# Kernel optimization log

Hardware: AMD Instinct MI355X
Metric: run time of the kernel (lower is better)

## Reference

```python
import jax, jax.numpy as jnp
import numpy as np

B, N = 4096, 128


def setup_inputs() -> dict:
    key = jax.random.key(0)
    X = jax.random.normal(key, (B, N, N), dtype=jnp.float32)
    # SPD batch: X X^T / N + eps*I guarantees strictly positive eigenvalues
    spd = jnp.einsum('bij,bkj->bik', X, X) / N + 1e-3 * jnp.eye(N, dtype=jnp.float32)[None]
    return {"input": spd}


def reference(input) -> jnp.ndarray:
    # Batched eigendecomposition (symmetric input -> eigh), then v @ diag(log e) @ v^T
    e, v = jnp.linalg.eigh(input)          # e: [B, N], v: [B, N, N]
    return jnp.einsum('bij,bj,bkj->bik', v, jnp.log(e), v)
```

## Files before the change

### kernel.cpp

```cpp
#include <hip/hip_runtime.h>
#include <hip/hip_bf16.h>
#include <math.h>

#define NM   128
#define PAD  132
#define PB   136

typedef __attribute__((ext_vector_type(8))) short bf16x8;
typedef __attribute__((ext_vector_type(4))) float f32x4;


__global__ __launch_bounds__(256,1)
void scale_kernel(const float* __restrict__ A, float* __restrict__ outY,
                  float* __restrict__ outM, float* __restrict__ lns)
{
    __shared__ __align__(16) float L[NM][PAD];
    __shared__ float rs[NM];
    __shared__ float s_inv;
    const int t = threadIdx.x;
    const long long b = blockIdx.x;
    const long long off = b << 14;
    for (int v = 0; v < 16; ++v) {
        int f = t + v*256;
        int row = f >> 5, c4 = (f & 31) << 2;
        *(float4*)&L[row][c4] = ((const float4*)(A + off))[f];
    }
    __syncthreads();
    if (t < NM) {
        float s = 0.f;
        for (int j = 0; j < NM; ++j) s += fabsf(L[t][j]);
        rs[t] = s;
    }
    __syncthreads();
    if (t < 64) {
        float m = fmaxf(rs[t], rs[t+64]);
        #pragma unroll
        for (int o = 32; o > 0; o >>= 1) m = fmaxf(m, __shfl_down(m, o, 64));
        if (t == 0) { s_inv = 1.0f/m; lns[b] = logf(m); }
    }
    __syncthreads();
    const float inv = s_inv;
    for (int v = 0; v < 16; ++v) {
        int f = t + v*256;
        int row = f >> 5, c4 = (f & 31) << 2;
        float4 x = *(const float4*)&L[row][c4];
        x.x *= inv; x.y *= inv; x.z *= inv; x.w *= inv;
        ((float4*)(outY + off))[f] = x;
        ((float4*)(outM + off))[f] = x;
    }
}

__global__ __launch_bounds__(256,1)
void rescale_kernel(const float* __restrict__ Sq, float* __restrict__ X,
                    float* __restrict__ M, float* __restrict__ lns)
{
    __shared__ __align__(16) float L[NM][PAD];
    __shared__ float rs[NM];
    __shared__ float s_g;
    const int t = threadIdx.x;
    const long long b = blockIdx.x;
    const long long off = b << 14;
    for (int v = 0; v < 16; ++v) {
        int f = t + v*256;
        int row = f >> 5, c4 = (f & 31) << 2;
        *(float4*)&L[row][c4] = ((const float4*)(Sq + off))[f];
    }
    __syncthreads();
    if (t < NM) {
        float s = 0.f;
        for (int j = 0; j < NM; ++j) s += fabsf(L[t][j]);
        rs[t] = s;
    }
    __syncthreads();
    if (t < 64) {
        float m = fmaxf(rs[t], rs[t+64]);
        #pragma unroll
        for (int o = 32; o > 0; o >>= 1) m = fmaxf(m, __shfl_down(m, o, 64));
        if (t == 0) { s_g = 1.0f/sqrtf(m); lns[b] = lns[b] + 0.5f*logf(m); }
    }
    __syncthreads();
    const float g = s_g;
    for (int v = 0; v < 16; ++v) {
        int f = t + v*256;
        float4 x = ((const float4*)(X + off))[f];
        x.x *= g; x.y *= g; x.z *= g; x.w *= g;
        ((float4*)(X + off))[f] = x;
        ((float4*)(M + off))[f] = x;
    }
}

__device__ __forceinline__ void tridec(int u, int &bi, int &bj) {
    int b = (int)(0.5f*(sqrtf(8.0f*(float)u + 1.0f) - 1.0f));
    while ((b+1)*(b+2)/2 <= u) ++b;
    while (b*(b+1)/2 > u) --b;
    bi = b; bj = u - b*(b+1)/2;
}

__global__ __launch_bounds__(512,1)
void gram_tri(const float* __restrict__ X, float* __restrict__ Out)
{
    __shared__ __align__(16) float LX[NM][PAD];
    const int t = threadIdx.x;
    const long long off = (long long)blockIdx.x << 14;
    for (int v = 0; v < 8; ++v) {
        int f = t + v*512;
        int row = f >> 5, c4 = (f & 31) << 2;
        *(float4*)&LX[row][c4] = ((const float4*)(X + off))[f];
    }
    __syncthreads();
    for (int u = t; u < 528; u += 512) {
        int bi, bj; tridec(u, bi, bj);
        const int r4 = bi << 2, c4 = bj << 2;
        float acc[4][4];
        #pragma unroll
        for (int i = 0; i < 4; ++i)
            #pragma unroll
            for (int j = 0; j < 4; ++j) acc[i][j] = 0.f;
        #pragma unroll 4
        for (int k = 0; k < NM; ++k) {
            float av[4], bv[4];
            *(float4*)av = *(const float4*)&LX[k][r4];
            *(float4*)bv = *(const float4*)&LX[k][c4];
            #pragma unroll
            for (int i = 0; i < 4; ++i)
                #pragma unroll
                for (int j = 0; j < 4; ++j) acc[i][j] = fmaf(av[i], bv[j], acc[i][j]);
        }
        #pragma unroll
        for (int i = 0; i < 4; ++i)
            *(float4*)&Out[off + (long long)(r4+i)*NM + c4] =
                make_float4(acc[i][0], acc[i][1], acc[i][2], acc[i][3]);
        if (bi != bj) {
            #pragma unroll
            for (int j = 0; j < 4; ++j)
                *(float4*)&Out[off + (long long)(c4+j)*NM + r4] =
                    make_float4(acc[0][j], acc[1][j], acc[2][j], acc[3][j]);
        }
    }
}

__device__ __forceinline__ void tri_p1_reg(const float (*LM)[PAD], const float (*LY)[PAD],
                                           int bi, int bj, float a15, float a05,
                                           float o[4][4])
{
    const int r4 = bi << 2, c4 = bj << 2;
    float acc[4][4];
    #pragma unroll
    for (int i = 0; i < 4; ++i)
        #pragma unroll
        for (int j = 0; j < 4; ++j) acc[i][j] = 0.f;
    #pragma unroll 4
    for (int k = 0; k < NM; ++k) {
        float av[4], bv[4];
        *(float4*)av = *(const float4*)&LY[k][r4];
        *(float4*)bv = *(const float4*)&LM[k][c4];
        #pragma unroll
        for (int i = 0; i < 4; ++i)
            #pragma unroll
            for (int j = 0; j < 4; ++j) acc[i][j] = fmaf(av[i], bv[j], acc[i][j]);
    }
    #pragma unroll
    for (int i = 0; i < 4; ++i)
        #pragma unroll
        for (int j = 0; j < 4; ++j)
            o[i][j] = a15*LY[r4+i][c4+j] - a05*acc[i][j];
    if (bi == bj) {
        #pragma unroll
        for (int i = 0; i < 4; ++i)
            #pragma unroll
            for (int j = 0; j < 4; ++j)
                if (j > i) { float s = 0.5f*(o[i][j] + o[j][i]); o[i][j] = s; o[j][i] = s; }
    }
}

__device__ __forceinline__ void tri_p2_lds(const float (*LM)[PAD], float (*LY)[PAD],
                                           int bi, int bj)
{
    const int r4 = bi << 2, c4 = bj << 2;
    float acc[4][4];
    #pragma unroll
    for (int i = 0; i < 4; ++i)
        #pragma unroll
        for (int j = 0; j < 4; ++j) acc[i][j] = 0.f;
    #pragma unroll 4
    for (int k = 0; k < NM; ++k) {
        float av[4], bv[4];
        *(float4*)av = *(const float4*)&LM[k][r4];
        *(float4*)bv = *(const float4*)&LM[k][c4];
        #pragma unroll
        for (int i = 0; i < 4; ++i)
            #pragma unroll
            for (int j = 0; j < 4; ++j) acc[i][j] = fmaf(av[i], bv[j], acc[i][j]);
    }
    #pragma unroll
    for (int i = 0; i < 4; ++i)
        *(float4*)&LY[r4+i][c4] = make_float4(acc[i][0], acc[i][1], acc[i][2], acc[i][3]);
    if (bi != bj) {
        #pragma unroll
        for (int j = 0; j < 4; ++j)
            *(float4*)&LY[c4+j][r4] = make_float4(acc[0][j], acc[1][j], acc[2][j], acc[3][j]);
    }
}

__device__ __forceinline__ void tri_p3_reg(const float (*LM)[PAD], const float (*LY)[PAD],
                                           int bi, int bj, float q, float o[4][4])
{
    const int r4 = bi << 2, c4 = bj << 2;
    float acc[4][4];
    #pragma unroll
    for (int i = 0; i < 4; ++i)
        #pragma unroll
        for (int j = 0; j < 4; ++j) acc[i][j] = 0.f;
    #pragma unroll 4
    for (int k = 0; k < NM; ++k) {
        float av[4], bv[4];
        *(float4*)av = *(const float4*)&LM[k][r4];
        *(float4*)bv = *(const float4*)&LY[k][c4];
        #pragma unroll
        for (int i = 0; i < 4; ++i)
            #pragma unroll
            for (int j = 0; j < 4; ++j) acc[i][j] = fmaf(av[i], bv[j], acc[i][j]);
    }
    #pragma unroll
    for (int i = 0; i < 4; ++i)
        #pragma unroll
        for (int j = 0; j < 4; ++j)
            o[i][j] = q*(9.f*LM[r4+i][c4+j] - 6.f*LY[r4+i][c4+j] + acc[i][j]);
    if (bi == bj) {
        #pragma unroll
        for (int i = 0; i < 4; ++i)
            #pragma unroll
            for (int j = 0; j < 4; ++j)
                if (j > i) { float s = 0.5f*(o[i][j] + o[j][i]); o[i][j] = s; o[j][i] = s; }
    }
}

__device__ __forceinline__ void tri_wb(float (*L)[PAD], int bi, int bj, const float o[4][4])
{
    const int r4 = bi << 2, c4 = bj << 2;
    #pragma unroll
    for (int i = 0; i < 4; ++i)
        *(float4*)&L[r4+i][c4] = make_float4(o[i][0], o[i][1], o[i][2], o[i][3]);
    if (bi != bj) {
        #pragma unroll
        for (int j = 0; j < 4; ++j)
            *(float4*)&L[c4+j][r4] = make_float4(o[0][j], o[1][j], o[2][j], o[3][j]);
    }
}

__global__ __launch_bounds__(512,1)
void ns_tri4(const float* __restrict__ Mp, const float* __restrict__ Yp,
             float* __restrict__ outM, float* __restrict__ outY, int niter)
{
    __shared__ __align__(16) float LM[NM][PAD];
    __shared__ __align__(16) float LY[NM][PAD];
    const int t = threadIdx.x;
    const long long off = (long long)blockIdx.x << 14;
    for (int v = 0; v < 8; ++v) {
        int f = t + v*512;
        int row = f >> 5, c4 = (f & 31) << 2;
        *(float4*)&LM[row][c4] = ((const float4*)(Mp + off))[f];
        *(float4*)&LY[row][c4] = ((const float4*)(Yp + off))[f];
    }
    __syncthreads();

    int b0i, b0j, b1i = -1, b1j = 0;
    tridec(t, b0i, b0j);
    if (t < 16) tridec(512 + t, b1i, b1j);

    const float cc = 1.5f, dd = sqrtf(1.5f);
    const float a15 = 1.5f*dd, a05 = 0.5f*dd, q = 0.25f*cc;
    float y0[4][4], y1[4][4], m0[4][4], m1[4][4];

    for (int it = 0; it < niter; ++it) {
        tri_p1_reg(LM, LY, b0i, b0j, a15, a05, y0);
        if (b1i >= 0) tri_p1_reg(LM, LY, b1i, b1j, a15, a05, y1);
        __syncthreads();
        tri_p2_lds(LM, LY, b0i, b0j);
        if (b1i >= 0) tri_p2_lds(LM, LY, b1i, b1j);
        __syncthreads();
        tri_p3_reg(LM, LY, b0i, b0j, q, m0);
        if (b1i >= 0) tri_p3_reg(LM, LY, b1i, b1j, q, m1);
        __syncthreads();
        tri_wb(LM, b0i, b0j, m0);
        tri_wb(LY, b0i, b0j, y0);
        if (b1i >= 0) { tri_wb(LM, b1i, b1j, m1); tri_wb(LY, b1i, b1j, y1); }
        __syncthreads();
    }

    for (int v = 0; v < 8; ++v) {
        int f = t + v*512;
        int row = f >> 5, c4 = (f & 31) << 2;
        ((float4*)(outM + off))[f] = *(const float4*)&LM[row][c4];
        ((float4*)(outY + off))[f] = *(const float4*)&LY[row][c4];
    }
}

__device__ __forceinline__ f32x4 mfma16(bf16x8 a, bf16x8 b, f32x4 c) {
    return __builtin_amdgcn_mfma_f32_16x16x32_bf16(a, b, c, 0, 0, 0);
}

__device__ __forceinline__ void splitbf(float x, unsigned short &h, unsigned short &l) {
    __hip_bfloat16 bh = __float2bfloat16(x);
    float r = x - __bfloat162float(bh);
    __hip_bfloat16 bl = __float2bfloat16(r);
    h = *(unsigned short*)&bh;
    l = *(unsigned short*)&bl;
}

__device__ __forceinline__ float ldsM(const unsigned short* __restrict__ H,
                                      const unsigned short* __restrict__ L,
                                      int row, int col) {
    unsigned int uh = ((unsigned int)H[row*PB + col]) << 16;
    unsigned int ul = ((unsigned int)L[row*PB + col]) << 16;
    return __uint_as_float(uh) + __uint_as_float(ul);
}

__device__ __forceinline__ bf16x8 ldfrag(const unsigned short* __restrict__ a,
                                         int rb, int lane, int kc) {
    int row = rb*16 + (lane & 15);
    int col = kc*32 + ((lane >> 4) & 3)*8;
    return *(const bf16x8*)(a + row*PB + col);
}

__device__ __forceinline__ f32x4 symdiag(f32x4 a, int lane) {
    const int g = (lane >> 4) & 3, j = lane & 15;
    const int rp = j & 3;
    f32x4 out;
    #pragma unroll
    for (int r = 0; r < 4; ++r) {
        int lp = 4*g + r + ((j >> 2) << 4);
        float t0 = __shfl(a[0], lp, 64);
        float t1 = __shfl(a[1], lp, 64);
        float t2 = __shfl(a[2], lp, 64);
        float t3 = __shfl(a[3], lp, 64);
        float tv = (rp == 0) ? t0 : (rp == 1) ? t1 : (rp == 2) ? t2 : t3;
        out[r] = 0.5f*(a[r] + tv);
    }
    return out;
}

__device__ __forceinline__ void st_split(unsigned short* __restrict__ H,
                                         unsigned short* __restrict__ L,
                                         int Tr, int Tc, int lane, f32x4 o) {
    int col = Tc*16 + (lane & 15);
    int rb  = Tr*16 + ((lane >> 4) & 3)*4;
    #pragma unroll
    for (int r = 0; r < 4; ++r) {
        unsigned short h, l;
        splitbf(o[r], h, l);
        H[(rb+r)*PB + col] = h;
        L[(rb+r)*PB + col] = l;
        if (Tr != Tc) { H[col*PB + rb + r] = h; L[col*PB + rb + r] = l; }
    }
}

__device__ __forceinline__ void stg_sym(float* __restrict__ out, long long off,
                                        int Tr, int Tc, int lane, f32x4 o) {
    int col = Tc*16 + (lane & 15);
    int rb  = Tr*16 + ((lane >> 4) & 3)*4;
    #pragma unroll
    for (int r = 0; r < 4; ++r)
        out[off + (long long)(rb+r)*NM + col] = o[r];
    if (Tr != Tc)
        *(f32x4*)&out[off + (long long)col*NM + rb] = o;
}

__device__ __forceinline__ f32x4 yepi(const unsigned short* __restrict__ Yh,
                                      const unsigned short* __restrict__ Yl,
                                      int Tr, int Tc, int lane, f32x4 a,
                                      float a15, float a05) {
    int col = Tc*16 + (lane & 15);
    int rb  = Tr*16 + ((lane >> 4) & 3)*4;
    f32x4 o;
    #pragma unroll
    for (int r = 0; r < 4; ++r)
        o[r] = a15*ldsM(Yh, Yl, rb+r, col) - a05*a[r];
    if (Tr == Tc) o = symdiag(o, lane);
    return o;
}

__device__ __forceinline__ f32x4 mepi(const unsigned short* __restrict__ Mh,
                                      const unsigned short* __restrict__ Ml,
                                      const unsigned short* __restrict__ Th,
                                      const unsigned short* __restrict__ Tl,
                                      int Tr, int Tc, int lane, f32x4 a, float q) {
    int col = Tc*16 + (lane & 15);
    int rb  = Tr*16 + ((lane >> 4) & 3)*4;
    f32x4 o;
    #pragma unroll
    for (int r = 0; r < 4; ++r)
        o[r] = q*(9.f*ldsM(Mh, Ml, rb+r, col) - 6.f*ldsM(Th, Tl, rb+r, col) + a[r]);
    if (Tr == Tc) o = symdiag(o, lane);
    return o;
}

__device__ __forceinline__ f32x4 pepi(const unsigned short* __restrict__ Ph,
                                      const unsigned short* __restrict__ Pl,
                                      int Tr, int Tc, int lane, f32x4 a,
                                      float s1, float s2, float dadd) {
    int col = Tc*16 + (lane & 15);
    int rb  = Tr*16 + ((lane >> 4) & 3)*4;
    f32x4 o;
    #pragma unroll
    for (int r = 0; r < 4; ++r)
        o[r] = s1*a[r] - s2*ldsM(Ph, Pl, rb+r, col) + ((rb+r) == col ? dadd : 0.f);
    if (Tr == Tc) o = symdiag(o, lane);
    return o;
}

template<int W>
struct TS16 {
    static constexpr int P  = W >> 2;
    static constexpr int Q  = W & 3;
    static constexpr int R0 = P;
    static constexpr int R1 = 7 - P;
    static constexpr int N  = (Q == 0) ? 3 : 2;
    static constexpr int g(int i)  { return 4*i + Q; }
    static constexpr int tr(int i) { return g(i) <= R0 ? R0 : R1; }
    static constexpr int tc(int i) { return g(i) <= R0 ? g(i) : g(i) - R0 - 1; }
};

template<int W>
__device__ __forceinline__ void tri16_gemm(const unsigned short* __restrict__ Ah,
                                           const unsigned short* __restrict__ Al,
                                           const unsigned short* __restrict__ Bh,
                                           const unsigned short* __restrict__ Bl,
                                           int lane, f32x4* acc) {
    using TS = TS16<W>;
    #pragma unroll
    for (int kc = 0; kc < 4; ++kc) {
        bf16x8 a0h = ldfrag(Ah, TS::R0, lane, kc), a0l = ldfrag(Al, TS::R0, lane, kc);
        bf16x8 a1h = ldfrag(Ah, TS::R1, lane, kc), a1l = ldfrag(Al, TS::R1, lane, kc);
        #pragma unroll
        for (int i = 0; i < TS::N; ++i) {
            const int r = TS::tr(i), c = TS::tc(i);
            bf16x8 bh = ldfrag(Bh, c, lane, kc), bl = ldfrag(Bl, c, lane, kc);
            bf16x8 ah = (r == TS::R0) ? a0h : a1h;
            bf16x8 al = (r == TS::R0) ? a0l : a1l;
            acc[i] = mfma16(ah, bh, acc[i]);
            acc[i] = mfma16(ah, bl, acc[i]);
            acc[i] = mfma16(al, bh, acc[i]);
        }
    }
}

template<int W>
__device__ __forceinline__ void ns_fused_body16(
    unsigned short* Mh, unsigned short* Ml,
    unsigned short* Yh, unsigned short* Yl,
    float* outY, long long off, int lane, int niter)
{
    using TS = TS16<W>;
    constexpr int NT_ = TS::N;
    const f32x4 z = {0.f, 0.f, 0.f, 0.f};
    f32x4 acc[NT_], yv[NT_];

    for (int j = 0; j < niter; ++j) {
        const int last = (j == niter-1);
        const float cc = (j < niter-3) ? 1.5f : ((j == niter-3) ? 1.116f : 1.0f);
        const float dd = sqrtf(cc);
        const float a15 = 1.5f*dd, a05 = 0.5f*dd;

        #pragma unroll
        for (int i = 0; i < NT_; ++i) acc[i] = z;
        tri16_gemm<W>(Yh, Yl, Mh, Ml, lane, acc);
        #pragma unroll
        for (int i = 0; i < NT_; ++i)
            yv[i] = yepi(Yh, Yl, TS::tr(i), TS::tc(i), lane, acc[i], a15, a05);

        if (last) {
            #pragma unroll
            for (int i = 0; i < NT_; ++i)
                stg_sym(outY, off, TS::tr(i), TS::tc(i), lane, yv[i]);
            return;
        }
        __syncthreads();

        #pragma unroll
        for (int i = 0; i < NT_; ++i) acc[i] = z;
        tri16_gemm<W>(Mh, Ml, Mh, Ml, lane, acc);
        #pragma unroll
        for (int i = 0; i < NT_; ++i)
            st_split(Yh, Yl, TS::tr(i), TS::tc(i), lane, acc[i]);
        __syncthreads();

        #pragma unroll
        for (int i = 0; i < NT_; ++i) acc[i] = z;
        tri16_gemm<W>(Mh, Ml, Yh, Yl, lane, acc);
        const float q = 0.25f*cc;
        #pragma unroll
        for (int i = 0; i < NT_; ++i)
            acc[i] = mepi(Mh, Ml, Yh, Yl, TS::tr(i), TS::tc(i), lane, acc[i], q);
        __syncthreads();

        #pragma unroll
        for (int i = 0; i < NT_; ++i)
            st_split(Mh, Ml, TS::tr(i), TS::tc(i), lane, acc[i]);
        #pragma unroll
        for (int i = 0; i < NT_; ++i)
            st_split(Yh, Yl, TS::tr(i), TS::tc(i), lane, yv[i]);
        __syncthreads();
    }
}

__global__ __launch_bounds__(1024,1)
void ns_fused(const float* __restrict__ Mp, const float* __restrict__ Yp,
              float* __restrict__ outY, int niter)
{
    __shared__ __align__(16) unsigned short pool[4*NM*PB];
    unsigned short* Mh = pool;
    unsigned short* Ml = pool + NM*PB;
    unsigned short* Yh = pool + 2*NM*PB;
    unsigned short* Yl = pool + 3*NM*PB;

    const int t = threadIdx.x;
    const long long off = (long long)blockIdx.x << 14;
    for (int v = 0; v < 4; ++v) {
        int f = t + v*1024;
        int row = f >> 5, c4 = (f & 31) << 2;
        float4 x = ((const float4*)(Mp + off))[f];
        ushort4 h, l;
        splitbf(x.x, h.x, l.x); splitbf(x.y, h.y, l.y);
        splitbf(x.z, h.z, l.z); splitbf(x.w, h.w, l.w);
        *(ushort4*)&Mh[row*PB + c4] = h;
        *(ushort4*)&Ml[row*PB + c4] = l;
        x = ((const float4*)(Yp + off))[f];
        splitbf(x.x, h.x, l.x); splitbf(x.y, h.y, l.y);
        splitbf(x.z, h.z, l.z); splitbf(x.w, h.w, l.w);
        *(ushort4*)&Yh[row*PB + c4] = h;
        *(ushort4*)&Yl[row*PB + c4] = l;
    }
    __syncthreads();

    const int lane = t & 63;
    const int w = t >> 6;
    switch (w) {
        case 0:  ns_fused_body16<0>(Mh,Ml,Yh,Yl,outY,off,lane,niter); break;
        case 1:  ns_fused_body16<1>(Mh,Ml,Yh,Yl,outY,off,lane,niter); break;
        case 2:  ns_fused_body16<2>(Mh,Ml,Yh,Yl,outY,off,lane,niter); break;
        case 3:  ns_fused_body16<3>(Mh,Ml,Yh,Yl,outY,off,lane,niter); break;
        case 4:  ns_fused_body16<4>(Mh,Ml,Yh,Yl,outY,off,lane,niter); break;
        case 5:  ns_fused_body16<5>(Mh,Ml,Yh,Yl,outY,off,lane,niter); break;
        case 6:  ns_fused_body16<6>(Mh,Ml,Yh,Yl,outY,off,lane,niter); break;
        case 7:  ns_fused_body16<7>(Mh,Ml,Yh,Yl,outY,off,lane,niter); break;
        case 8:  ns_fused_body16<8>(Mh,Ml,Yh,Yl,outY,off,lane,niter); break;
        case 9:  ns_fused_body16<9>(Mh,Ml,Yh,Yl,outY,off,lane,niter); break;
        case 10: ns_fused_body16<10>(Mh,Ml,Yh,Yl,outY,off,lane,niter); break;
        case 11: ns_fused_body16<11>(Mh,Ml,Yh,Yl,outY,off,lane,niter); break;
        case 12: ns_fused_body16<12>(Mh,Ml,Yh,Yl,outY,off,lane,niter); break;
        case 13: ns_fused_body16<13>(Mh,Ml,Yh,Yl,outY,off,lane,niter); break;
        case 14: ns_fused_body16<14>(Mh,Ml,Yh,Yl,outY,off,lane,niter); break;
        default: ns_fused_body16<15>(Mh,Ml,Yh,Yl,outY,off,lane,niter); break;
    }
}

struct PolyCoefs {
    float a, bd;
    float s1, s2;
    float c0,c1,c2,c3,c4,c5;
    float f1, f2, f3;
};

template<int W>
__device__ __forceinline__ void poly_fused_body16(
    const unsigned short* Xh, const unsigned short* Xl,
    unsigned short* Ph, unsigned short* Pl,
    float* Out, long long off, int lane, PolyCoefs pc, float lnsb)
{
    using TS = TS16<W>;
    constexpr int NT_ = TS::N;
    const f32x4 z = {0.f, 0.f, 0.f, 0.f};
    f32x4 acc[NT_];

    for (int step = 0; step < 6; ++step) {
        #pragma unroll
        for (int i = 0; i < NT_; ++i) acc[i] = z;
        tri16_gemm<W>(Xh, Xl, Ph, Pl, lane, acc);
        float s3v;
        switch (step) {
            case 0: s3v = pc.c0; break;  case 1: s3v = pc.c1; break;
            case 2: s3v = pc.c2; break;  case 3: s3v = pc.c3; break;
            case 4: s3v = pc.c4; break;  default: s3v = pc.c5; break;
        }
        #pragma unroll
        for (int i = 0; i < NT_; ++i)
            acc[i] = pepi(Ph, Pl, TS::tr(i), TS::tc(i), lane, acc[i], pc.s1, pc.s2, s3v);
        __syncthreads();
        #pragma unroll
        for (int i = 0; i < NT_; ++i)
            st_split(Ph, Pl, TS::tr(i), TS::tc(i), lane, acc[i]);
        __syncthreads();
    }
    #pragma unroll
    for (int i = 0; i < NT_; ++i) acc[i] = z;
    tri16_gemm<W>(Xh, Xl, Ph, Pl, lane, acc);
    const float dadd = pc.f3 + lnsb;
    #pragma unroll
    for (int i = 0; i < NT_; ++i) {
        f32x4 o = pepi(Ph, Pl, TS::tr(i), TS::tc(i), lane, acc[i], pc.f1, pc.f2, dadd);
        stg_sym(Out, off, TS::tr(i), TS::tc(i), lane, o);
    }
}

__global__ __launch_bounds__(1024,1)
void poly_fused(const float* __restrict__ Xp, float* __restrict__ Out,
                const float* __restrict__ lns, PolyCoefs pc)
{
    __shared__ __align__(16) unsigned short pool[4*NM*PB];
    unsigned short* Xh = pool;
    unsigned short* Xl = pool + NM*PB;
    unsigned short* Ph = pool + 2*NM*PB;
    unsigned short* Pl = pool + 3*NM*PB;

    const int t = threadIdx.x;
    const long long b = blockIdx.x;
    const long long off = b << 14;
    for (int v = 0; v < 4; ++v) {
        int f = t + v*1024;
        int row = f >> 5, c4 = (f & 31) << 2;
        float4 x = ((const float4*)(Xp + off))[f];
        float4 p;
        p.x = pc.a*x.x + ((c4+0)==row ? pc.bd : 0.f);
        p.y = pc.a*x.y + ((c4+1)==row ? pc.bd : 0.f);
        p.z = pc.a*x.z + ((c4+2)==row ? pc.bd : 0.f);
        p.w = pc.a*x.w + ((c4+3)==row ? pc.bd : 0.f);
        ushort4 h, l;
        splitbf(x.x, h.x, l.x); splitbf(x.y, h.y, l.y);
        splitbf(x.z, h.z, l.z); splitbf(x.w, h.w, l.w);
        *(ushort4*)&Xh[row*PB + c4] = h;
        *(ushort4*)&Xl[row*PB + c4] = l;
        splitbf(p.x, h.x, l.x); splitbf(p.y, h.y, l.y);
        splitbf(p.z, h.z, l.z); splitbf(p.w, h.w, l.w);
        *(ushort4*)&Ph[row*PB + c4] = h;
        *(ushort4*)&Pl[row*PB + c4] = l;
    }
    __syncthreads();

    const float lnsb = lns[b];
    const int lane = t & 63;
    const int w = t >> 6;
    switch (w) {
        case 0:  poly_fused_body16<0>(Xh,Xl,Ph,Pl,Out,off,lane,pc,lnsb); break;
        case 1:  poly_fused_body16<1>(Xh,Xl,Ph,Pl,Out,off,lane,pc,lnsb); break;
        case 2:  poly_fused_body16<2>(Xh,Xl,Ph,Pl,Out,off,lane,pc,lnsb); break;
        case 3:  poly_fused_body16<3>(Xh,Xl,Ph,Pl,Out,off,lane,pc,lnsb); break;
        case 4:  poly_fused_body16<4>(Xh,Xl,Ph,Pl,Out,off,lane,pc,lnsb); break;
        case 5:  poly_fused_body16<5>(Xh,Xl,Ph,Pl,Out,off,lane,pc,lnsb); break;
        case 6:  poly_fused_body16<6>(Xh,Xl,Ph,Pl,Out,off,lane,pc,lnsb); break;
        case 7:  poly_fused_body16<7>(Xh,Xl,Ph,Pl,Out,off,lane,pc,lnsb); break;
        case 8:  poly_fused_body16<8>(Xh,Xl,Ph,Pl,Out,off,lane,pc,lnsb); break;
        case 9:  poly_fused_body16<9>(Xh,Xl,Ph,Pl,Out,off,lane,pc,lnsb); break;
        case 10: poly_fused_body16<10>(Xh,Xl,Ph,Pl,Out,off,lane,pc,lnsb); break;
        case 11: poly_fused_body16<11>(Xh,Xl,Ph,Pl,Out,off,lane,pc,lnsb); break;
        case 12: poly_fused_body16<12>(Xh,Xl,Ph,Pl,Out,off,lane,pc,lnsb); break;
        case 13: poly_fused_body16<13>(Xh,Xl,Ph,Pl,Out,off,lane,pc,lnsb); break;
        case 14: poly_fused_body16<14>(Xh,Xl,Ph,Pl,Out,off,lane,pc,lnsb); break;
        default: poly_fused_body16<15>(Xh,Xl,Ph,Pl,Out,off,lane,pc,lnsb); break;
    }
}

#define LDA  129
#define NT   512
#define MAX_SWEEPS 14

__global__ __launch_bounds__(NT, 1)
void logeig_jacobi(const float* __restrict__ in, float* __restrict__ out)
{
    __shared__ float A[NM][LDA];
    __shared__ float V[NM][LDA];
    __shared__ float rc[64], rs[64];
    __shared__ float logd[NM];
    __shared__ float roff[NT/64], rdia[NT/64];
    __shared__ int   s_done;

    const int t = threadIdx.x;
    const long long b = blockIdx.x;
    const float* __restrict__ Ain  = in  + (b << 14);
    float* __restrict__       Aout = out + (b << 14);

    for (int k = 0; k < (NM*NM)/NT; ++k) {
        int idx = t + k*NT;
        int i = idx >> 7, j = idx & 127;
        A[i][j] = Ain[idx];
        V[i][j] = (i == j) ? 1.0f : 0.0f;
    }
    __syncthreads();

    for (int sweep = 0; sweep < MAX_SWEEPS; ++sweep) {
        for (int r = 0; r < NM-1; ++r) {
            if (t < 64) {
                int m = t, p, q;
                if (m == 0) { p = NM-1; q = r; }
                else {
                    p = r + m;            if (p >= NM-1) p -= (NM-1);
                    q = r - m + (NM-1);   if (q >= NM-1) q -= (NM-1);
                }
                float app = A[p][p], aqq = A[q][q], apq = A[p][q];
                float c = 1.0f, s = 0.0f;
                if (fabsf(apq) > 1e-12f*(fabsf(app)+fabsf(aqq)) + 1e-32f) {
                    float tau = (aqq - app) * 0.5f / apq;
                    float tt  = 1.0f / (fabsf(tau) + sqrtf(fmaf(tau,tau,1.0f)));
                    tt = (tau < 0.0f) ? -tt : tt;
                    c = rsqrtf(fmaf(tt,tt,1.0f));
                    s = tt * c;
                }
                rc[m] = c; rs[m] = s;
            }
            __syncthreads();
            for (int k = 0; k < (2*64*NM)/NT; ++k) {
                int task = t + k*NT;
                int i   = task & 127;
                int m   = (task >> 7) & 63;
                int isV = task >> 13;
                int p, q;
                if (m == 0) { p = NM-1; q = r; }
                else {
                    p = r + m;            if (p >= NM-1) p -= (NM-1);
                    q = r - m + (NM-1);   if (q >= NM-1) q -= (NM-1);
                }
                float c = rc[m], s = rs[m];
                if (isV == 0) {
                    float x = A[i][p], y = A[i][q];
                    A[i][p] = c*x - s*y;
                    A[i][q] = s*x + c*y;
                } else {
                    float x = V[i][p], y = V[i][q];
                    V[i][p] = c*x - s*y;
                    V[i][q] = s*x + c*y;
                }
            }
            __syncthreads();
            for (int k = 0; k < (64*NM)/NT; ++k) {
                int task = t + k*NT;
                int j = task & 127;
                int m = task >> 7;
                int p, q;
                if (m == 0) { p = NM-1; q = r; }
                else {
                    p = r + m;            if (p >= NM-1) p -= (NM-1);
                    q = r - m + (NM-1);   if (q >= NM-1) q -= (NM-1);
                }
                float c = rc[m], s = rs[m];
                float x = A[p][j], y = A[q][j];
                A[p][j] = c*x - s*y;
                A[q][j] = s*x + c*y;
            }
            __syncthreads();
        }
        float off2 = 0.0f, dia2 = 0.0f;
        for (int k = 0; k < (NM*NM)/NT; ++k) {
            int idx = t + k*NT;
            int i = idx >> 7, j = idx & 127;
            float v = A[i][j];
            if (i == j) dia2 += v*v; else off2 += v*v;
        }
        #pragma unroll
        for (int o = 32; o > 0; o >>= 1) {
            off2 += __shfl_down(off2, o, 64);
            dia2 += __shfl_down(dia2, o, 64);
        }
        if ((t & 63) == 0) { roff[t >> 6] = off2; rdia[t >> 6] = dia2; }
        __syncthreads();
        if (t == 0) {
            float o2 = 0.0f, d2 = 0.0f;
            for (int w = 0; w < NT/64; ++w) { o2 += roff[w]; d2 += rdia[w]; }
            s_done = (o2 <= 1e-13f * d2) ? 1 : 0;
        }
        __syncthreads();
        if (s_done) break;
    }

    if (t < NM) logd[t] = logf(fmaxf(A[t][t], 1e-12f));
    __syncthreads();
    for (int kk = 0; kk < (NM*NM)/NT; ++kk) {
        int idx = t + kk*NT;
        int i = idx >> 7, k = idx & 127;
        A[i][k] = V[i][k] * logd[k];
    }
    __syncthreads();
    {
        int i  = t >> 2;
        int jb = t & 3;
        float acc[32];
        #pragma unroll
        for (int jj = 0; jj < 32; ++jj) acc[jj] = 0.0f;
        for (int kk = 0; kk < NM; ++kk) {
            int k = (kk + jb) & 127;
            float w = A[i][k];
            #pragma unroll
            for (int jj = 0; jj < 32; ++jj)
                acc[jj] = fmaf(w, V[jb*32 + jj][k], acc[jj]);
        }
        #pragma unroll
        for (int jj = 0; jj < 32; ++jj)
            Aout[i*NM + jb*32 + jj] = acc[jj];
    }
}

static void cheb_log_power(double lo, double up, int deg, double* p)
{
    const int NC = deg + 1;
    const int MN = 64;
    double mid = 0.5*(lo+up), hw = 0.5*(up-lo);
    double cc[32];
    for (int j = 0; j < NC; ++j) {
        double s = 0.0;
        for (int m = 0; m < MN; ++m) {
            double th = M_PI*(m+0.5)/MN;
            s += log(mid + hw*cos(th)) * cos(j*th);
        }
        cc[j] = 2.0*s/MN;
    }
    double Tp[32] = {0}, Tc[32] = {0}, Tn[32];
    for (int j = 0; j < NC; ++j) p[j] = 0.0;
    Tp[0] = 1.0;  p[0] += 0.5*cc[0];
    Tc[1] = 1.0;  p[1] += cc[1];
    for (int k = 2; k <= deg; ++k) {
        for (int j = 0; j < NC; ++j) Tn[j] = -Tp[j];
        for (int j = 1; j < NC; ++j) Tn[j] += 2.0*Tc[j-1];
        for (int j = 0; j < NC; ++j) { p[j] += cc[k]*Tn[j]; Tp[j] = Tc[j]; Tc[j] = Tn[j]; }
    }
}

extern "C" void kernel_launch(void* const* d_in, const int* in_sizes, int n_in,
                              void* d_out, int out_size, void* d_ws, size_t ws_size,
                              hipStream_t stream) {
    const float* in = (const float*)d_in[0];
    float* out = (float*)d_out;
    const int batch = in_sizes[0] >> 14;
    const size_t matBytes = (size_t)batch * NM * NM * 4;
    const size_t need = matBytes + (size_t)batch * 4;

    if (ws_size < need) {
        logeig_jacobi<<<batch, NT, 0, stream>>>(in, out);
        return;
    }

    float* Mbuf = (float*)d_ws;
    float* lns  = (float*)((char*)d_ws + matBytes);

    scale_kernel<<<batch, 256, 0, stream>>>(in, out, Mbuf, lns);
    gram_tri<<<batch, 512, 0, stream>>>(out, Mbuf);
    rescale_kernel<<<batch, 256, 0, stream>>>(Mbuf, out, Mbuf, lns);

    ns_tri4<<<batch, 512, 0, stream>>>(Mbuf, out, Mbuf, out, 4);

    ns_fused<<<batch, 1024, 0, stream>>>(Mbuf, out, out, 8);
    ns_fused<<<batch, 1024, 0, stream>>>(out,  out, out, 8);
    ns_fused<<<batch, 1024, 0, stream>>>(out,  out, out, 6);

    const double lo = 0.25, up = 1.002;
    const double mid = 0.5*(lo+up), hw = 0.5*(up-lo);
    double p[9];
    cheb_log_power(lo, up, 8, p);

    PolyCoefs pc;
    pc.a  = (float)(p[8]/hw);
    pc.bd = (float)(p[7] - p[8]*mid/hw);
    pc.s1 = (float)(1.0/hw);
    pc.s2 = (float)(mid/hw);
    pc.c0 = (float)p[6]; pc.c1 = (float)p[5]; pc.c2 = (float)p[4];
    pc.c3 = (float)p[3]; pc.c4 = (float)p[2]; pc.c5 = (float)p[1];
    pc.f1 = (float)(8.0/hw);
    pc.f2 = (float)(8.0*mid/hw);
    pc.f3 = (float)(8.0*p[0]);

    poly_fused<<<batch, 1024, 0, stream>>>(out, out, lns, pc);
}
```

Before: 7.207 ms.

## Run first Newton-Schulz stage with int8 MFMA using three-way fixed-point split

Adds an ns_i8 kernel that encodes M and Y as 24-bit fixed-point values split into three int8 planes in LDS. The triangular Newton-Schulz GEMMs then run as eight int8 16x16x64 MFMAs per tile, reconstructed in fp32. It replaces ns_tri4 for the first four iterations when the int8 MFMA builtin is available. The aim is to use the higher int8 matrix throughput in place of the bf16 split path. In exchange it adds fixed-point quantization, which assumes values stay within a bounded range, plus extra packing and unpacking work.

```diff
diff --git a/kernel.cpp b/kernel.cpp
--- a/kernel.cpp
+++ b/kernel.cpp
@@ -5,9 +5,17 @@
 #define NM   128
 #define PAD  132
 #define PB   136
+#define PBI  144
 
 typedef __attribute__((ext_vector_type(8))) short bf16x8;
 typedef __attribute__((ext_vector_type(4))) float f32x4;
+typedef __attribute__((ext_vector_type(4))) int   i32x4;
+
+#if defined(__has_builtin)
+#if __has_builtin(__builtin_amdgcn_mfma_i32_16x16x64_i8)
+#define HAVE_I8MFMA 1
+#endif
+#endif
 
 
 __global__ __launch_bounds__(256,1)
@@ -659,6 +667,259 @@
         default: poly_fused_body16<15>(Xh,Xl,Ph,Pl,Out,off,lane,pc,lnsb); break;
     }
 }
+
+#if HAVE_I8MFMA
+
+__device__ __forceinline__ i32x4 mfma8(i32x4 a, i32x4 b, i32x4 c) {
+    return __builtin_amdgcn_mfma_i32_16x16x64_i8(a, b, c, 0, 0, 0);
+}
+
+__device__ __forceinline__ void spliti(float x, int &h, int &m, int &l) {
+    int xi = __float2int_rn(x * 2097152.0f);
+    l = (int)(signed char)(xi & 255);
+    int r1 = (xi - l) >> 8;
+    m = (int)(signed char)(r1 & 255);
+    h = (r1 - m) >> 8;
+}
+
+__device__ __forceinline__ void pack4i(float4 x, unsigned &uh, unsigned &um, unsigned &ul) {
+    float v[4] = {x.x, x.y, x.z, x.w};
+    uh = um = ul = 0;
+    #pragma unroll
+    for (int i = 0; i < 4; ++i) {
+        int h, m, l;
+        spliti(v[i], h, m, l);
+        uh |= ((unsigned)(h & 255)) << (8*i);
+        um |= ((unsigned)(m & 255)) << (8*i);
+        ul |= ((unsigned)(l & 255)) << (8*i);
+    }
+}
+
+__device__ __forceinline__ float recLDS(const signed char* __restrict__ H,
+                                        const signed char* __restrict__ Md,
+                                        const signed char* __restrict__ L,
+                                        int row, int col) {
+    int v = ((int)H[row*PBI + col] << 16) + ((int)Md[row*PBI + col] << 8)
+          + (int)L[row*PBI + col];
+    return (float)v * 4.76837158203125e-7f;
+}
+
+__device__ __forceinline__ f32x4 rec4(i32x4 g0, i32x4 g1, i32x4 g2, i32x4 g3) {
+    f32x4 r;
+    #pragma unroll
+    for (int i = 0; i < 4; ++i)
+        r[i] = (float)g0[i]*9.765625e-4f
+             + (float)g1[i]*3.814697265625e-6f
+             + (float)g2[i]*1.4901161193847656e-8f
+             + (float)g3[i]*5.8207660913467407e-11f;
+    return r;
+}
+
+__device__ __forceinline__ i32x4 ldfrag8(const signed char* __restrict__ p,
+                                         int rb, int lane, int kc) {
+    int row = rb*16 + (lane & 15);
+    int col = kc*64 + ((lane >> 4) & 3)*16;
+    return *(const i32x4*)(p + row*PBI + col);
+}
+
+__device__ __forceinline__ void st_spliti(signed char* __restrict__ H,
+                                          signed char* __restrict__ Md,
+                                          signed char* __restrict__ L,
+                                          int Tr, int Tc, int lane, f32x4 o) {
+    int col = Tc*16 + (lane & 15);
+    int rb  = Tr*16 + ((lane >> 4) & 3)*4;
+    #pragma unroll
+    for (int r = 0; r < 4; ++r) {
+        int h, m, l;
+        spliti(o[r], h, m, l);
+        H[(rb+r)*PBI + col] = (signed char)h;
+        Md[(rb+r)*PBI + col] = (signed char)m;
+        L[(rb+r)*PBI + col] = (signed char)l;
+        if (Tr != Tc) {
+            H[col*PBI + rb + r] = (signed char)h;
+            Md[col*PBI + rb + r] = (signed char)m;
+            L[col*PBI + rb + r] = (signed char)l;
+        }
+    }
+}
+
+template<int W>
+struct TS8 {
+    static constexpr int P  = W & 3;
+    static constexpr int R0 = P;
+    static constexpr int R1 = 7 - P;
+    static constexpr int H  = W >> 2;
+    static constexpr int N  = (10 - H) / 2;
+    static constexpr int tr(int i) { int g = 2*i + H; return g <= R0 ? R0 : R1; }
+    static constexpr int tc(int i) { int g = 2*i + H; return g <= R0 ? g : g - R0 - 1; }
+};
+
+template<int W>
+__device__ __forceinline__ void tri8_gemm_i8(
+    const signed char* __restrict__ Ah, const signed char* __restrict__ Am,
+    const signed char* __restrict__ Al,
+    const signed char* __restrict__ Bh, const signed char* __restrict__ Bm,
+    const signed char* __restrict__ Bl,
+    int lane, i32x4* g0, i32x4* g1, i32x4* g2, i32x4* g3)
+{
+    using TS = TS8<W>;
+    #pragma unroll
+    for (int kc = 0; kc < 2; ++kc) {
+        i32x4 a0h = ldfrag8(Ah, TS::R0, lane, kc);
+        i32x4 a0m = ldfrag8(Am, TS::R0, lane, kc);
+        i32x4 a0l = ldfrag8(Al, TS::R0, lane, kc);
+        i32x4 a1h = ldfrag8(Ah, TS::R1, lane, kc);
+        i32x4 a1m = ldfrag8(Am, TS::R1, lane, kc);
+        i32x4 a1l = ldfrag8(Al, TS::R1, lane, kc);
+        #pragma unroll
+        for (int i = 0; i < TS::N; ++i) {
+            const int r = TS::tr(i), c = TS::tc(i);
+            i32x4 bh = ldfrag8(Bh, c, lane, kc);
+            i32x4 bm = ldfrag8(Bm, c, lane, kc);
+            i32x4 bl = ldfrag8(Bl, c, lane, kc);
+            i32x4 ah = (r == TS::R0) ? a0h : a1h;
+            i32x4 am = (r == TS::R0) ? a0m : a1m;
+            i32x4 al = (r == TS::R0) ? a0l : a1l;
+            g0[i] = mfma8(ah, bh, g0[i]);
+            g1[i] = mfma8(ah, bm, g1[i]);
+            g1[i] = mfma8(am, bh, g1[i]);
+            g2[i] = mfma8(ah, bl, g2[i]);
+            g2[i] = mfma8(am, bm, g2[i]);
+            g2[i] = mfma8(al, bh, g2[i]);
+            g3[i] = mfma8(am, bl, g3[i]);
+            g3[i] = mfma8(al, bm, g3[i]);
+        }
+    }
+}
+
+template<int W>
+__device__ __forceinline__ void ns_i8_body(
+    signed char* Mh, signed char* Mm, signed char* Ml,
+    signed char* Yh, signed char* Ym, signed char* Yl,
+    float* outM, float* outY, long long off, int lane, int niter)
+{
+    using TS = TS8<W>;
+    constexpr int NT_ = TS::N;
+    const i32x4 zi = {0, 0, 0, 0};
+    i32x4 g0[NT_], g1[NT_], g2[NT_], g3[NT_];
+    f32x4 yv[NT_], mv[NT_];
+    const float cc = 1.5f, dd = sqrtf(1.5f);
+    const float a15 = 1.5f*dd, a05 = 0.5f*dd, q = 0.25f*cc;
+
+    for (int j = 0; j < niter; ++j) {
+        const int last = (j == niter-1);
+
+        #pragma unroll
+        for (int i = 0; i < NT_; ++i) { g0[i]=zi; g1[i]=zi; g2[i]=zi; g3[i]=zi; }
+        tri8_gemm_i8<W>(Yh,Ym,Yl, Mh,Mm,Ml, lane, g0,g1,g2,g3);
+        #pragma unroll
+        for (int i = 0; i < NT_; ++i) {
+            f32x4 a = rec4(g0[i], g1[i], g2[i], g3[i]);
+            int Tr = TS::tr(i), Tc = TS::tc(i);
+            int col = Tc*16 + (lane & 15);
+            int rb  = Tr*16 + ((lane >> 4) & 3)*4;
+            f32x4 o;
+            #pragma unroll
+            for (int r = 0; r < 4; ++r)
+                o[r] = a15*recLDS(Yh, Ym, Yl, rb+r, col) - a05*a[r];
+            if (Tr == Tc) o = symdiag(o, lane);
+            yv[i] = o;
+        }
+        __syncthreads();
+
+        #pragma unroll
+        for (int i = 0; i < NT_; ++i) { g0[i]=zi; g1[i]=zi; g2[i]=zi; g3[i]=zi; }
+        tri8_gemm_i8<W>(Mh,Mm,Ml, Mh,Mm,Ml, lane, g0,g1,g2,g3);
+        #pragma unroll
+        for (int i = 0; i < NT_; ++i) {
+            f32x4 tv = rec4(g0[i], g1[i], g2[i], g3[i]);
+            st_spliti(Yh, Ym, Yl, TS::tr(i), TS::tc(i), lane, tv);
+        }
+        __syncthreads();
+
+        #pragma unroll
+        for (int i = 0; i < NT_; ++i) { g0[i]=zi; g1[i]=zi; g2[i]=zi; g3[i]=zi; }
+        tri8_gemm_i8<W>(Mh,Mm,Ml, Yh,Ym,Yl, lane, g0,g1,g2,g3);
+        #pragma unroll
+        for (int i = 0; i < NT_; ++i) {
+            f32x4 a = rec4(g0[i], g1[i], g2[i], g3[i]);
+            int Tr = TS::tr(i), Tc = TS::tc(i);
+            int col = Tc*16 + (lane & 15);
+            int rb  = Tr*16 + ((lane >> 4) & 3)*4;
+            f32x4 o;
+            #pragma unroll
+            for (int r = 0; r < 4; ++r)
+                o[r] = q*(9.f*recLDS(Mh, Mm, Ml, rb+r, col)
+                        - 6.f*recLDS(Yh, Ym, Yl, rb+r, col) + a[r]);
+            if (Tr == Tc) o = symdiag(o, lane);
+            mv[i] = o;
+        }
+        __syncthreads();
+
+        if (last) {
+            #pragma unroll
+            for (int i = 0; i < NT_; ++i)
+                stg_sym(outY, off, TS::tr(i), TS::tc(i), lane, yv[i]);
+            #pragma unroll
+            for (int i = 0; i < NT_; ++i)
+                stg_sym(outM, off, TS::tr(i), TS::tc(i), lane, mv[i]);
+        } else {
+            #pragma unroll
+            for (int i = 0; i < NT_; ++i)
+                st_spliti(Mh, Mm, Ml, TS::tr(i), TS::tc(i), lane, mv[i]);
+            #pragma unroll
+            for (int i = 0; i < NT_; ++i)
+                st_spliti(Yh, Ym, Yl, TS::tr(i), TS::tc(i), lane, yv[i]);
+            __syncthreads();
+        }
+    }
+}
+
+__global__ __launch_bounds__(512,1)
+void ns_i8(const float* __restrict__ Mp, const float* __restrict__ Yp,
+           float* __restrict__ outM, float* __restrict__ outY, int niter)
+{
+    __shared__ __align__(16) signed char pool8[6*NM*PBI];
+    signed char* Mh = pool8;
+    signed char* Mm = pool8 + 1*NM*PBI;
+    signed char* Ml = pool8 + 2*NM*PBI;
+    signed char* Yh = pool8 + 3*NM*PBI;
+    signed char* Ym = pool8 + 4*NM*PBI;
+    signed char* Yl = pool8 + 5*NM*PBI;
+
+    const int t = threadIdx.x;
+    const long long off = (long long)blockIdx.x << 14;
+    for (int v = 0; v < 8; ++v) {
+        int f = t + v*512;
+        int row = f >> 5, c4 = (f & 31) << 2;
+        unsigned uh, um, ul;
+        float4 x = ((const float4*)(Mp + off))[f];
+        pack4i(x, uh, um, ul);
+        *(unsigned*)&Mh[row*PBI + c4] = uh;
+        *(unsigned*)&Mm[row*PBI + c4] = um;
+        *(unsigned*)&Ml[row*PBI + c4] = ul;
+        x = ((const float4*)(Yp + off))[f];
+        pack4i(x, uh, um, ul);
+        *(unsigned*)&Yh[row*PBI + c4] = uh;
+        *(unsigned*)&Ym[row*PBI + c4] = um;
+        *(unsigned*)&Yl[row*PBI + c4] = ul;
+    }
+    __syncthreads();
+
+    const int lane = t & 63;
+    const int w = t >> 6;
+    switch (w) {
+        case 0:  ns_i8_body<0>(Mh,Mm,Ml,Yh,Ym,Yl,outM,outY,off,lane,niter); break;
+        case 1:  ns_i8_body<1>(Mh,Mm,Ml,Yh,Ym,Yl,outM,outY,off,lane,niter); break;
+        case 2:  ns_i8_body<2>(Mh,Mm,Ml,Yh,Ym,Yl,outM,outY,off,lane,niter); break;
+        case 3:  ns_i8_body<3>(Mh,Mm,Ml,Yh,Ym,Yl,outM,outY,off,lane,niter); break;
+        case 4:  ns_i8_body<4>(Mh,Mm,Ml,Yh,Ym,Yl,outM,outY,off,lane,niter); break;
+        case 5:  ns_i8_body<5>(Mh,Mm,Ml,Yh,Ym,Yl,outM,outY,off,lane,niter); break;
+        case 6:  ns_i8_body<6>(Mh,Mm,Ml,Yh,Ym,Yl,outM,outY,off,lane,niter); break;
+        default: ns_i8_body<7>(Mh,Mm,Ml,Yh,Ym,Yl,outM,outY,off,lane,niter); break;
+    }
+}
+#endif
 
 #define LDA  129
 #define NT   512
@@ -844,7 +1105,11 @@
     gram_tri<<<batch, 512, 0, stream>>>(out, Mbuf);
     rescale_kernel<<<batch, 256, 0, stream>>>(Mbuf, out, Mbuf, lns);
 
+#if HAVE_I8MFMA
+    ns_i8<<<batch, 512, 0, stream>>>(Mbuf, out, Mbuf, out, 4);
+#else
     ns_tri4<<<batch, 512, 0, stream>>>(Mbuf, out, Mbuf, out, 4);
+#endif
 
     ns_fused<<<batch, 1024, 0, stream>>>(Mbuf, out, out, 8);
     ns_fused<<<batch, 1024, 0, stream>>>(out,  out, out, 8);
```

After: 7.207 ms. Within noise of the previous version (-0.0%).
